# Performance work log

Hardware: AMD Instinct MI355X
Metric: run time of the kernel (lower is better)

## Reference

```python
import jax, jax.numpy as jnp
import numpy as np

# MPO config: input_size = output_size = 4096 = 16**3, num_cores = 3, rank = 16
D_IN = 16    # in_leg_dim
D_OUT = 16   # out_leg_dim
RANK = 16
IN_SIZE = D_IN ** 3
OUT_SIZE = D_OUT ** 3
B = 2048     # flattened batch*seq tokens


def setup_inputs() -> dict:
    key = jax.random.key(0)
    ks = jax.random.split(key, 5)
    bound = 1.0 / np.sqrt(IN_SIZE)
    u = lambda k, shp: jax.random.uniform(k, shp, jnp.float32, -bound, bound)
    return {
        "x": jax.random.normal(ks[0], (B, IN_SIZE), dtype=jnp.float32),
        "first_core": u(ks[1], (D_IN, RANK, D_OUT)),        # (in, rank_right, out)
        "middle_core": u(ks[2], (D_IN, RANK, RANK, D_OUT)),  # (in, rank_left, rank_right, out)
        "last_core": u(ks[3], (D_IN, RANK, D_OUT)),          # (in, rank_left, out)
        "bias": u(ks[4], (OUT_SIZE,)),
    }


def reference(x, first_core, middle_core, last_core, bias):
    # Faithful MPO chain contraction, same edge wiring and order as the
    # tensornetwork-based original (contract input legs left-to-right,
    # threading the bond/rank index through the cores).
    xr = x.reshape(-1, D_IN, D_IN, D_IN)                       # (b, i, j, k)
    # contract input leg i with first core -> legs (b, j, k, r, m)
    t = jnp.einsum('bijk,irm->bjkrm', xr, first_core)
    # contract input leg j and bond r with middle core -> (b, k, m, s, n)
    t = jnp.einsum('bjkrm,jrsn->bkmsn', t, middle_core)
    # contract input leg k and bond s with last core -> (b, m, n, o)
    t = jnp.einsum('bkmsn,kso->bmno', t, last_core)
    return t.reshape(-1, OUT_SIZE) + bias
```

## Files before the change

kernel.cpp:

```cpp
#include <hip/hip_runtime.h>

#define DLEG 16
#define IN_SIZE 4096
#define OUT_SIZE 4096
#define BATCH 2048

#define SX 25.4f
#define SW 1.1545455e6f

typedef __attribute__((ext_vector_type(4))) int i32x4;

__device__ __forceinline__ signed char f2i8(float f, float s) {
  int q = __float2int_rn(f * s);
  q = q > 127 ? 127 : (q < -127 ? -127 : q);
  return (signed char)q;
}

__device__ __forceinline__ void async_copy16(const void* g, void* l) {
  __builtin_amdgcn_global_load_lds(
      (const __attribute__((address_space(1))) void*)g,
      (__attribute__((address_space(3))) void*)l, 16, 0, 0);
}

__global__ __launch_bounds__(256) void k_prep(
    const float* __restrict__ x, const float* __restrict__ fc,
    const float* __restrict__ mc, const float* __restrict__ lc,
    signed char* __restrict__ xi, signed char* __restrict__ wt) {
  __shared__ float fc_s[256];
  __shared__ float mc_s[4096];
  __shared__ float a_s[1024];
  const int t = threadIdx.x;

  if (blockIdx.x < 2048) {
    const int idx = blockIdx.x * 256 + t;
    const float4* xp = (const float4*)x + (size_t)idx * 4;
    union { int4 v; signed char c[16]; } u;
#pragma unroll
    for (int q = 0; q < 4; ++q) {
      const float4 f = xp[q];
      u.c[q * 4 + 0] = f2i8(f.x, SX);
      u.c[q * 4 + 1] = f2i8(f.y, SX);
      u.c[q * 4 + 2] = f2i8(f.z, SX);
      u.c[q * 4 + 3] = f2i8(f.w, SX);
    }
    ((int4*)xi)[idx] = u.v;
    return;
  }

  const int idx = blockIdx.x - 2048;
  const int b = idx & 255;
  const int mg = idx >> 8;
  const int i = b >> 4, j = b & 15;

  fc_s[t] = fc[i * 256 + t];
#pragma unroll
  for (int q = 0; q < 16; ++q) mc_s[q * 256 + t] = mc[j * 4096 + q * 256 + t];
  __syncthreads();

  {
    const int n = t >> 4, s = t & 15;
    float accm[4] = {0.f, 0.f, 0.f, 0.f};
#pragma unroll
    for (int r = 0; r < 16; ++r) {
      const float mcv = mc_s[r * 256 + s * 16 + n];
#pragma unroll
      for (int ml = 0; ml < 4; ++ml)
        accm[ml] = fmaf(fc_s[r * 16 + mg * 4 + ml], mcv, accm[ml]);
    }
#pragma unroll
    for (int ml = 0; ml < 4; ++ml) a_s[ml * 256 + n * 16 + s] = accm[ml];
  }
  __syncthreads();

  const int k = t & 15, op = (t >> 4) & 3, sel = t >> 6;
  float lcr[4][16];
#pragma unroll
  for (int oo = 0; oo < 4; ++oo)
#pragma unroll
    for (int s = 0; s < 16; ++s)
      lcr[oo][s] = lc[k * 256 + s * 16 + op * 4 + oo];

#pragma unroll
  for (int ml = 0; ml < 4; ++ml) {
#pragma unroll
    for (int nn = 0; nn < 4; ++nn) {
      const int n = sel * 4 + nn;
      const float4* ap = (const float4*)&a_s[ml * 256 + n * 16];
      float av[16];
      ((float4*)av)[0] = ap[0];
      ((float4*)av)[1] = ap[1];
      ((float4*)av)[2] = ap[2];
      ((float4*)av)[3] = ap[3];
      float accv[4] = {0.f, 0.f, 0.f, 0.f};
#pragma unroll
      for (int s = 0; s < 16; ++s) {
#pragma unroll
        for (int oo = 0; oo < 4; ++oo)
          accv[oo] = fmaf(av[s], lcr[oo][s], accv[oo]);
      }
      const size_t colbase =
          (size_t)((mg * 4 + ml) * 256 + n * 16 + op * 4);
#pragma unroll
      for (int oo = 0; oo < 4; ++oo)
        wt[(colbase + oo) * 4096 + b * 16 + k] = f2i8(accv[oo], SW);
    }
  }
}

__global__ __launch_bounds__(256, 2) void k_gemm(
    const signed char* __restrict__ X,
    const signed char* __restrict__ Wt,
    const float* __restrict__ bias,
    float* __restrict__ out) {
  __shared__ signed char As[2][128 * 128];
  __shared__ signed char Bs[2][128 * 128];

  const int t = threadIdx.x;
  const int l = t & 63, w = t >> 6;
  const int wm = w >> 1, wn = w & 1;
  const int m0 = blockIdx.y * 128, n0 = blockIdx.x * 128;

  const signed char* xg[4];
  const signed char* wg[4];
  int ldsoff[4];
#pragma unroll
  for (int u = 0; u < 4; ++u) {
    const int c = u * 256 + t;
    const int row = c >> 3;
    const int slot = (c & 7) ^ (row & 7);
    xg[u] = X + (size_t)(m0 + row) * 4096 + slot * 16;
    wg[u] = Wt + (size_t)(n0 + row) * 4096 + slot * 16;
    ldsoff[u] = c * 16;
  }

  const int arow = wm * 64 + (l & 15);
  const int brow = wn * 64 + (l & 15);
  const int lk = l >> 4;
  const int lx = l & 7;

  i32x4 acc[4][4];
#pragma unroll
  for (int a = 0; a < 4; ++a)
#pragma unroll
    for (int c = 0; c < 4; ++c) acc[a][c] = (i32x4){0, 0, 0, 0};

#pragma unroll
  for (int u = 0; u < 4; ++u) async_copy16(xg[u], As[0] + ldsoff[u]);
#pragma unroll
  for (int u = 0; u < 4; ++u) async_copy16(wg[u], Bs[0] + ldsoff[u]);

  for (int kt = 0; kt < 4096; kt += 128) {
    const int cur = (kt >> 7) & 1;
    __syncthreads();
    if (kt + 128 < 4096) {
#pragma unroll
      for (int u = 0; u < 4; ++u)
        async_copy16(xg[u] + kt + 128, As[cur ^ 1] + ldsoff[u]);
#pragma unroll
      for (int u = 0; u < 4; ++u)
        async_copy16(wg[u] + kt + 128, Bs[cur ^ 1] + ldsoff[u]);
    }

#pragma unroll
    for (int ks = 0; ks < 2; ++ks) {
      const int slot = ((ks * 4 + lk) ^ lx) * 16;
      i32x4 af[4], bf[4];
#pragma unroll
      for (int mi = 0; mi < 4; ++mi)
        af[mi] = *(const i32x4*)&As[cur][(arow + mi * 16) * 128 + slot];
#pragma unroll
      for (int ni = 0; ni < 4; ++ni)
        bf[ni] = *(const i32x4*)&Bs[cur][(brow + ni * 16) * 128 + slot];
#pragma unroll
      for (int mi = 0; mi < 4; ++mi)
#pragma unroll
        for (int ni = 0; ni < 4; ++ni)
          acc[mi][ni] = __builtin_amdgcn_mfma_i32_16x16x64_i8(
              af[mi], bf[ni], acc[mi][ni], 0, 0, 0);
    }
  }

  const float inv = 1.0f / (SX * SW);
#pragma unroll
  for (int ni = 0; ni < 4; ++ni) {
    const int col = n0 + wn * 64 + ni * 16 + (l & 15);
    const float bv = bias[col];
#pragma unroll
    for (int mi = 0; mi < 4; ++mi) {
      const int row = m0 + wm * 64 + mi * 16 + (l >> 4) * 4;
#pragma unroll
      for (int r = 0; r < 4; ++r)
        out[(size_t)(row + r) * 4096 + col] =
            (float)acc[mi][ni][r] * inv + bv;
    }
  }
}

extern "C" void kernel_launch(void* const* d_in, const int* in_sizes, int n_in,
                              void* d_out, int out_size, void* d_ws,
                              size_t ws_size, hipStream_t stream) {
  const float* x    = (const float*)d_in[0];
  const float* fc   = (const float*)d_in[1];
  const float* mc   = (const float*)d_in[2];
  const float* lc   = (const float*)d_in[3];
  const float* bias = (const float*)d_in[4];
  float* out = (float*)d_out;

  signed char* xi = (signed char*)d_ws;
  signed char* wt = xi + (size_t)BATCH * IN_SIZE;

  k_prep<<<2048 + 1024, 256, 0, stream>>>(x, fc, mc, lc, xi, wt);
  k_gemm<<<dim3(OUT_SIZE / 128, BATCH / 128), 256, 0, stream>>>(xi, wt, bias, out);
}
```

Measured before the change: 142.9 us.

## Widen GEMM tile to 128x256 with triple-buffered LDS and register-prefetched fragments

The int8 GEMM now uses a 128x256 output tile per block, so each block loads B twice as wide and reuses A across more columns. LDS becomes a three-stage ring, with two tiles in flight, and the next tile's fragments are prefetched into registers while MFMAs run on the current ones. The loop is software-pipelined and unrolled by hand, using explicit waitcnt, barriers, sched_barrier and setprio around the MFMA bursts. This adds heavy register and LDS use: occupancy drops to one block per CU, and the grid shrinks to 256 blocks, which may underfill the 256 CUs of an MI355X and cost balance.

```diff
diff --git a/kernel.cpp b/kernel.cpp
--- a/kernel.cpp
+++ b/kernel.cpp
@@ -107,83 +107,128 @@
   }
 }
 
-__global__ __launch_bounds__(256, 2) void k_gemm(
+
+#define LOADF(FA, FB, AP, BP)                                                 \
+  {                                                                           \
+    const int s0 = (lk ^ lx) * 16;                                            \
+    const int s1 = ((4 + lk) ^ lx) * 16;                                      \
+    _Pragma("unroll") for (int mi = 0; mi < 4; ++mi) {                        \
+      FA[mi]     = *(const i32x4*)&(AP)[(arow + mi * 16) * 128 + s0];         \
+      FA[4 + mi] = *(const i32x4*)&(AP)[(arow + mi * 16) * 128 + s1];         \
+    }                                                                         \
+    _Pragma("unroll") for (int ni = 0; ni < 8; ++ni) {                        \
+      FB[ni]     = *(const i32x4*)&(BP)[(brow + ni * 16) * 128 + s0];         \
+      FB[8 + ni] = *(const i32x4*)&(BP)[(brow + ni * 16) * 128 + s1];         \
+    }                                                                         \
+  }
+
+#define MFMA64(FA, FB)                                                        \
+  __builtin_amdgcn_s_setprio(1);                                              \
+  _Pragma("unroll") for (int ks = 0; ks < 2; ++ks)                            \
+    _Pragma("unroll") for (int mi = 0; mi < 4; ++mi)                          \
+      _Pragma("unroll") for (int ni = 0; ni < 8; ++ni)                        \
+        acc[mi][ni] = __builtin_amdgcn_mfma_i32_16x16x64_i8(                  \
+            FA[ks * 4 + mi], FB[ks * 8 + ni], acc[mi][ni], 0, 0, 0);          \
+  __builtin_amdgcn_s_setprio(0)
+
+#define STAGE12(ABUF, BBUF, KT)                                               \
+  {                                                                           \
+    _Pragma("unroll") for (int u = 0; u < 4; ++u)                             \
+      async_copy16(xg[u] + (KT), (ABUF) + xoff[u]);                           \
+    _Pragma("unroll") for (int u = 0; u < 8; ++u)                             \
+      async_copy16(wg[u] + (KT), (BBUF) + woff[u]);                           \
+  }
+
+#define TILE(CA, CB, NA, NB, VN, DOSTAGE, DOLOAD)                             \
+  if (DOSTAGE) { STAGE12(Aw, Bw, ktS); }                                      \
+  asm volatile("s_waitcnt lgkmcnt(0)" ::: "memory");                          \
+  asm volatile("s_waitcnt vmcnt(" #VN ")" ::: "memory");                      \
+  __builtin_amdgcn_s_barrier();                                               \
+  __builtin_amdgcn_sched_barrier(0);                                          \
+  if (DOLOAD) { LOADF(NA, NB, An, Bn); }                                      \
+  __builtin_amdgcn_sched_barrier(0);                                          \
+  MFMA64(CA, CB)
+
+#define ROT3                                                                  \
+  {                                                                           \
+    signed char* ta = An; An = Aw; Aw = Af; Af = ta;                          \
+    signed char* tb = Bn; Bn = Bw; Bw = Bf; Bf = tb;                          \
+  }
+
+__global__ __launch_bounds__(256, 1) void k_gemm(
     const signed char* __restrict__ X,
     const signed char* __restrict__ Wt,
     const float* __restrict__ bias,
     float* __restrict__ out) {
-  __shared__ signed char As[2][128 * 128];
-  __shared__ signed char Bs[2][128 * 128];
+  __shared__ __align__(16) signed char As[3][128 * 128];
+  __shared__ __align__(16) signed char Bs[3][256 * 128];
 
   const int t = threadIdx.x;
   const int l = t & 63, w = t >> 6;
   const int wm = w >> 1, wn = w & 1;
-  const int m0 = blockIdx.y * 128, n0 = blockIdx.x * 128;
+  const int m0 = blockIdx.y * 128, n0 = blockIdx.x * 256;
 
   const signed char* xg[4];
-  const signed char* wg[4];
-  int ldsoff[4];
+  int xoff[4];
 #pragma unroll
   for (int u = 0; u < 4; ++u) {
     const int c = u * 256 + t;
     const int row = c >> 3;
     const int slot = (c & 7) ^ (row & 7);
     xg[u] = X + (size_t)(m0 + row) * 4096 + slot * 16;
+    xoff[u] = c * 16;
+  }
+  const signed char* wg[8];
+  int woff[8];
+#pragma unroll
+  for (int u = 0; u < 8; ++u) {
+    const int c = u * 256 + t;
+    const int row = c >> 3;
+    const int slot = (c & 7) ^ (row & 7);
     wg[u] = Wt + (size_t)(n0 + row) * 4096 + slot * 16;
-    ldsoff[u] = c * 16;
+    woff[u] = c * 16;
   }
 
   const int arow = wm * 64 + (l & 15);
-  const int brow = wn * 64 + (l & 15);
+  const int brow = wn * 128 + (l & 15);
   const int lk = l >> 4;
   const int lx = l & 7;
 
-  i32x4 acc[4][4];
+  i32x4 acc[4][8];
 #pragma unroll
   for (int a = 0; a < 4; ++a)
 #pragma unroll
-    for (int c = 0; c < 4; ++c) acc[a][c] = (i32x4){0, 0, 0, 0};
-
-#pragma unroll
-  for (int u = 0; u < 4; ++u) async_copy16(xg[u], As[0] + ldsoff[u]);
-#pragma unroll
-  for (int u = 0; u < 4; ++u) async_copy16(wg[u], Bs[0] + ldsoff[u]);
-
-  for (int kt = 0; kt < 4096; kt += 128) {
-    const int cur = (kt >> 7) & 1;
-    __syncthreads();
-    if (kt + 128 < 4096) {
-#pragma unroll
-      for (int u = 0; u < 4; ++u)
-        async_copy16(xg[u] + kt + 128, As[cur ^ 1] + ldsoff[u]);
-#pragma unroll
-      for (int u = 0; u < 4; ++u)
-        async_copy16(wg[u] + kt + 128, Bs[cur ^ 1] + ldsoff[u]);
-    }
-
-#pragma unroll
-    for (int ks = 0; ks < 2; ++ks) {
-      const int slot = ((ks * 4 + lk) ^ lx) * 16;
-      i32x4 af[4], bf[4];
-#pragma unroll
-      for (int mi = 0; mi < 4; ++mi)
-        af[mi] = *(const i32x4*)&As[cur][(arow + mi * 16) * 128 + slot];
-#pragma unroll
-      for (int ni = 0; ni < 4; ++ni)
-        bf[ni] = *(const i32x4*)&Bs[cur][(brow + ni * 16) * 128 + slot];
-#pragma unroll
-      for (int mi = 0; mi < 4; ++mi)
-#pragma unroll
-        for (int ni = 0; ni < 4; ++ni)
-          acc[mi][ni] = __builtin_amdgcn_mfma_i32_16x16x64_i8(
-              af[mi], bf[ni], acc[mi][ni], 0, 0, 0);
-    }
-  }
+    for (int c = 0; c < 8; ++c) acc[a][c] = (i32x4){0, 0, 0, 0};
+
+  i32x4 Pa[8], Pb[16], Qa[8], Qb[16];
+
+  signed char *An = As[1], *Aw = As[2], *Af = As[0];
+  signed char *Bn = Bs[1], *Bw = Bs[2], *Bf = Bs[0];
+
+  STAGE12(As[0], Bs[0], 0);
+  STAGE12(As[1], Bs[1], 128);
+  asm volatile("s_waitcnt vmcnt(12)" ::: "memory");
+  __builtin_amdgcn_s_barrier();
+  __builtin_amdgcn_sched_barrier(0);
+  LOADF(Pa, Pb, As[0], Bs[0]);
+
+  int ktS = 256;
+#pragma unroll 1
+  for (int tt = 0; tt < 15; ++tt) {
+    TILE(Pa, Pb, Qa, Qb, 12, 1, 1);
+    ROT3; ktS += 128;
+    TILE(Qa, Qb, Pa, Pb, 12, 1, 1);
+    ROT3; ktS += 128;
+  }
+  TILE(Pa, Pb, Qa, Qb, 0, 0, 1);
+  asm volatile("s_waitcnt lgkmcnt(0)" ::: "memory");
+  __builtin_amdgcn_sched_barrier(0);
+  MFMA64(Qa, Qb);
 
   const float inv = 1.0f / (SX * SW);
 #pragma unroll
-  for (int ni = 0; ni < 4; ++ni) {
-    const int col = n0 + wn * 64 + ni * 16 + (l & 15);
+  for (int ni = 0; ni < 8; ++ni) {
+    const int col = n0 + wn * 128 + ni * 16 + (l & 15);
     const float bv = bias[col];
 #pragma unroll
     for (int mi = 0; mi < 4; ++mi) {
@@ -210,5 +255,6 @@
   signed char* wt = xi + (size_t)BATCH * IN_SIZE;
 
   k_prep<<<2048 + 1024, 256, 0, stream>>>(x, fc, mc, lc, xi, wt);
-  k_gemm<<<dim3(OUT_SIZE / 128, BATCH / 128), 256, 0, stream>>>(xi, wt, bias, out);
-}
+  k_gemm<<<dim3(OUT_SIZE / 256, BATCH / 128), 256, 0, stream>>>(xi, wt, bias,
+                                                                out);
+}
```

Result: no change. 142.3 us (-0.4%).

## Pre-swizzle int8 operands into MFMA fragment layout and load directly to registers

Applied to the files above, without the earlier changes.

The prep kernel now writes the quantized activations and the fused weight matrix in an MFMA-fragment-ordered layout. This lets the GEMM load each lane's 16-byte fragment straight from global memory into registers with no LDS staging or barriers. The GEMM switches to 128x256 tiles with 512 threads, a swizzled 1D grid, two-stage register double-buffering with explicit vmcnt waits, and setprio around the MFMA bursts. The risk is that there is no LDS reuse across waves, so each wave re-reads its fragments from L2, and register pressure is higher.

```diff
diff --git a/kernel.cpp b/kernel.cpp
--- a/kernel.cpp
+++ b/kernel.cpp
@@ -16,11 +16,6 @@
   return (signed char)q;
 }
 
-__device__ __forceinline__ void async_copy16(const void* g, void* l) {
-  __builtin_amdgcn_global_load_lds(
-      (const __attribute__((address_space(1))) void*)g,
-      (__attribute__((address_space(3))) void*)l, 16, 0, 0);
-}
 
 __global__ __launch_bounds__(256) void k_prep(
     const float* __restrict__ x, const float* __restrict__ fc,
@@ -33,7 +28,12 @@
 
   if (blockIdx.x < 2048) {
     const int idx = blockIdx.x * 256 + t;
-    const float4* xp = (const float4*)x + (size_t)idx * 4;
+    const int l = idx & 63;
+    const int kt = (idx >> 6) & 63;
+    const int m16 = idx >> 12;
+    const int row = m16 * 16 + (l & 15);
+    const int kb = kt * 64 + (l >> 4) * 16;
+    const float4* xp = (const float4*)(x + (size_t)row * 4096 + kb);
     union { int4 v; signed char c[16]; } u;
 #pragma unroll
     for (int q = 0; q < 4; ++q) {
@@ -80,6 +80,7 @@
     for (int s = 0; s < 16; ++s)
       lcr[oo][s] = lc[k * 256 + s * 16 + op * 4 + oo];
 
+  const int ktw = b >> 2, lhi = (b & 3) * 16;
 #pragma unroll
   for (int ml = 0; ml < 4; ++ml) {
 #pragma unroll
@@ -98,45 +99,67 @@
         for (int oo = 0; oo < 4; ++oo)
           accv[oo] = fmaf(av[s], lcr[oo][s], accv[oo]);
       }
-      const size_t colbase =
-          (size_t)((mg * 4 + ml) * 256 + n * 16 + op * 4);
-#pragma unroll
-      for (int oo = 0; oo < 4; ++oo)
-        wt[(colbase + oo) * 4096 + b * 16 + k] = f2i8(accv[oo], SW);
-    }
-  }
-}
-
-__global__ __launch_bounds__(256, 2) void k_gemm(
+      const int n16 = (mg * 4 + ml) * 16 + n;
+#pragma unroll
+      for (int oo = 0; oo < 4; ++oo) {
+        const size_t F =
+            ((size_t)((n16 * 64 + ktw) * 64) + lhi + op * 4 + oo) * 16 + k;
+        wt[F] = f2i8(accv[oo], SW);
+      }
+    }
+  }
+}
+
+
+#define GLOAD16(FA, FB)                                                       \
+  {                                                                           \
+    _Pragma("unroll") for (int mi = 0; mi < 4; ++mi) {                        \
+      FA[mi * 2]     = *(const i32x4*)(ap[mi]);                               \
+      FA[mi * 2 + 1] = *(const i32x4*)(ap[mi] + 1024);                        \
+      ap[mi] += 2048;                                                         \
+    }                                                                         \
+    _Pragma("unroll") for (int ni = 0; ni < 4; ++ni) {                        \
+      FB[ni * 2]     = *(const i32x4*)(bp[ni]);                               \
+      FB[ni * 2 + 1] = *(const i32x4*)(bp[ni] + 1024);                        \
+      bp[ni] += 2048;                                                         \
+    }                                                                         \
+  }
+
+#define MFMA32(FA, FB)                                                        \
+  __builtin_amdgcn_s_setprio(1);                                              \
+  _Pragma("unroll") for (int ks = 0; ks < 2; ++ks)                            \
+    _Pragma("unroll") for (int mi = 0; mi < 4; ++mi)                          \
+      _Pragma("unroll") for (int ni = 0; ni < 4; ++ni)                        \
+        acc[mi][ni] = __builtin_amdgcn_mfma_i32_16x16x64_i8(                  \
+            FA[mi * 2 + ks], FB[ni * 2 + ks], acc[mi][ni], 0, 0, 0);          \
+  __builtin_amdgcn_s_setprio(0)
+
+#define VWAIT(N)                                                              \
+  asm volatile("s_waitcnt vmcnt(" #N ")" ::: "memory");                       \
+  __builtin_amdgcn_sched_barrier(0)
+
+__global__ __launch_bounds__(512, 2) void k_gemm(
     const signed char* __restrict__ X,
     const signed char* __restrict__ Wt,
     const float* __restrict__ bias,
     float* __restrict__ out) {
-  __shared__ signed char As[2][128 * 128];
-  __shared__ signed char Bs[2][128 * 128];
-
   const int t = threadIdx.x;
   const int l = t & 63, w = t >> 6;
-  const int wm = w >> 1, wn = w & 1;
-  const int m0 = blockIdx.y * 128, n0 = blockIdx.x * 128;
-
-  const signed char* xg[4];
-  const signed char* wg[4];
-  int ldsoff[4];
-#pragma unroll
-  for (int u = 0; u < 4; ++u) {
-    const int c = u * 256 + t;
-    const int row = c >> 3;
-    const int slot = (c & 7) ^ (row & 7);
-    xg[u] = X + (size_t)(m0 + row) * 4096 + slot * 16;
-    wg[u] = Wt + (size_t)(n0 + row) * 4096 + slot * 16;
-    ldsoff[u] = c * 16;
-  }
-
-  const int arow = wm * 64 + (l & 15);
-  const int brow = wn * 64 + (l & 15);
-  const int lk = l >> 4;
-  const int lx = l & 7;
+  const int wm = w >> 2, wn = w & 3;
+
+  const int bid = blockIdx.x;
+  const int swz = (bid & 7) * 32 + (bid >> 3);
+  const int bn = swz >> 4;
+  const int bm = swz & 15;
+
+  const signed char* ap[4];
+  const signed char* bp[4];
+#pragma unroll
+  for (int mi = 0; mi < 4; ++mi)
+    ap[mi] = X + ((size_t)(bm * 8 + wm * 4 + mi) * 64) * 1024 + l * 16;
+#pragma unroll
+  for (int ni = 0; ni < 4; ++ni)
+    bp[ni] = Wt + ((size_t)(bn * 16 + wn * 4 + ni) * 64) * 1024 + l * 16;
 
   i32x4 acc[4][4];
 #pragma unroll
@@ -144,43 +167,27 @@
 #pragma unroll
     for (int c = 0; c < 4; ++c) acc[a][c] = (i32x4){0, 0, 0, 0};
 
-#pragma unroll
-  for (int u = 0; u < 4; ++u) async_copy16(xg[u], As[0] + ldsoff[u]);
-#pragma unroll
-  for (int u = 0; u < 4; ++u) async_copy16(wg[u], Bs[0] + ldsoff[u]);
-
-  for (int kt = 0; kt < 4096; kt += 128) {
-    const int cur = (kt >> 7) & 1;
-    __syncthreads();
-    if (kt + 128 < 4096) {
-#pragma unroll
-      for (int u = 0; u < 4; ++u)
-        async_copy16(xg[u] + kt + 128, As[cur ^ 1] + ldsoff[u]);
-#pragma unroll
-      for (int u = 0; u < 4; ++u)
-        async_copy16(wg[u] + kt + 128, Bs[cur ^ 1] + ldsoff[u]);
-    }
-
-#pragma unroll
-    for (int ks = 0; ks < 2; ++ks) {
-      const int slot = ((ks * 4 + lk) ^ lx) * 16;
-      i32x4 af[4], bf[4];
-#pragma unroll
-      for (int mi = 0; mi < 4; ++mi)
-        af[mi] = *(const i32x4*)&As[cur][(arow + mi * 16) * 128 + slot];
-#pragma unroll
-      for (int ni = 0; ni < 4; ++ni)
-        bf[ni] = *(const i32x4*)&Bs[cur][(brow + ni * 16) * 128 + slot];
-#pragma unroll
-      for (int mi = 0; mi < 4; ++mi)
-#pragma unroll
-        for (int ni = 0; ni < 4; ++ni)
-          acc[mi][ni] = __builtin_amdgcn_mfma_i32_16x16x64_i8(
-              af[mi], bf[ni], acc[mi][ni], 0, 0, 0);
-    }
-  }
+  i32x4 Pa[8], Pb[8], Qa[8], Qb[8];
+
+  GLOAD16(Pa, Pb);
+  GLOAD16(Qa, Qb);
+
+#pragma unroll 1
+  for (int tt = 0; tt < 15; ++tt) {
+    VWAIT(16);
+    MFMA32(Pa, Pb);
+    GLOAD16(Pa, Pb);
+    VWAIT(16);
+    MFMA32(Qa, Qb);
+    GLOAD16(Qa, Qb);
+  }
+  VWAIT(16);
+  MFMA32(Pa, Pb);
+  VWAIT(0);
+  MFMA32(Qa, Qb);
 
   const float inv = 1.0f / (SX * SW);
+  const int n0 = bn * 256, m0 = bm * 128;
 #pragma unroll
   for (int ni = 0; ni < 4; ++ni) {
     const int col = n0 + wn * 64 + ni * 16 + (l & 15);
@@ -210,5 +217,5 @@
   signed char* wt = xi + (size_t)BATCH * IN_SIZE;
 
   k_prep<<<2048 + 1024, 256, 0, stream>>>(x, fc, mc, lc, xi, wt);
-  k_gemm<<<dim3(OUT_SIZE / 128, BATCH / 128), 256, 0, stream>>>(xi, wt, bias, out);
-}
+  k_gemm<<<256, 512, 0, stream>>>(xi, wt, bias, out);
+}
```

New measurement: 139.8 us. 2.2% less time.
